# Kernel tuning notes

Measured on AMD Instinct MI355X. Metric: run time of the kernel, lower is better.

The kernel has to match this reference:

```python
import jax, jax.numpy as jnp
import numpy as np

B, IN, H, U = 65536, 128, 256, 256

def lecun_tanh(x):
    return 1.7159 * jnp.tanh(0.666 * x)

def _xavier(key, shape):
    fan_out, fan_in = shape
    limit = np.sqrt(6.0 / (fan_in + fan_out))
    return jax.random.uniform(key, shape, jnp.float32, -limit, limit)

def setup_inputs() -> dict:
    key = jax.random.key(0)
    ks = jax.random.split(key, 12)
    return {
        "input": jax.random.normal(ks[0], (B, IN), jnp.float32),
        "hx": jax.random.normal(ks[1], (B, H), jnp.float32),
        "ts": jax.random.uniform(ks[2], (B, 1), jnp.float32),
        # backbone Linear(IN+H -> U)
        "Wb": _xavier(ks[3], (U, IN + H)),
        "bb": jnp.zeros((U,), jnp.float32),
        # ff1, ff2, time_a, time_b: Linear(U -> H)
        "W1": _xavier(ks[4], (H, U)),
        "b1": jnp.zeros((H,), jnp.float32),
        "W2": _xavier(ks[5], (H, U)),
        "b2": jnp.zeros((H,), jnp.float32),
        "Wa": _xavier(ks[6], (H, U)),
        "ba": jnp.zeros((H,), jnp.float32),
        "Wt": _xavier(ks[7], (H, U)),
        "bt": jnp.zeros((H,), jnp.float32),
    }

def reference(input, hx, ts, Wb, bb, W1, b1, W2, b2, Wa, ba, Wt, bt):
    # x = cat([input, hx]) -> backbone MLP (1 layer, LeCun tanh)
    x = jnp.concatenate([input, hx], axis=1)          # [B, IN+H]
    x = lecun_tanh(x @ Wb.T + bb)                     # [B, U]
    ff1 = jnp.tanh(x @ W1.T + b1)                     # [B, H]
    ff2 = jnp.tanh(x @ W2.T + b2)
    t_a = x @ Wa.T + ba
    t_b = x @ Wt.T + bt
    t_interp = jax.nn.sigmoid(t_a * ts + t_b)         # ts broadcasts [B,1]
    new_hidden = ff1 * (1.0 - t_interp) + t_interp * ff2
    return new_hidden
```

## Files before the change

### kernel.cpp

```cpp
#include <hip/hip_runtime.h>

typedef float v4f __attribute__((ext_vector_type(4)));
typedef short v8s __attribute__((ext_vector_type(8)));

#define BM 64

__device__ __forceinline__ unsigned short f2bf(float f) {
    union { float f; unsigned u; } v; v.f = f;
    unsigned u = v.u;
    u += 0x7FFFu + ((u >> 16) & 1u);
    return (unsigned short)(u >> 16);
}

__device__ __forceinline__ unsigned cvt_pk_bf16(float lo, float hi) {
    unsigned r;
    asm("v_cvt_pk_bf16_f32 %0, %1, %2" : "=v"(r) : "v"(lo), "v"(hi));
    return r;
}

#define LDS_BARRIER() do {                                        \
    asm volatile("s_waitcnt lgkmcnt(0)" ::: "memory");            \
    __builtin_amdgcn_s_barrier();                                 \
    __builtin_amdgcn_sched_barrier(0);                            \
} while (0)

#define SB() __builtin_amdgcn_sched_barrier(0)

__device__ __forceinline__ float fast_exp2(float x) {
#if __has_builtin(__builtin_amdgcn_exp2f)
    return __builtin_amdgcn_exp2f(x);
#else
    return exp2f(x);
#endif
}
__device__ __forceinline__ float fast_rcp(float x) {
#if __has_builtin(__builtin_amdgcn_rcpf)
    return __builtin_amdgcn_rcpf(x);
#else
    return 1.0f / x;
#endif
}
__device__ __forceinline__ float fast_tanh(float y) {
    float t = fast_exp2(y * 2.885390081777927f);
    return (t - 1.0f) * fast_rcp(t + 1.0f);
}
__device__ __forceinline__ float fast_sigmoid(float z) {
    float t = fast_exp2(-1.4426950408889634f * z);
    return fast_rcp(1.0f + t);
}

__global__ void prep_pack(const float* __restrict__ Wb, const float* __restrict__ W1,
                          const float* __restrict__ W2, const float* __restrict__ Wa,
                          const float* __restrict__ Wt, unsigned short* __restrict__ ws)
{
    int e = blockIdx.x * 256 + threadIdx.x;
    if (e >= 360448) return;
    const float* src; int K; int base;
    if (e < 98304)       { src = Wb; K = 384; base = 0; }
    else if (e < 163840) { src = W1; K = 256; base = 98304; }
    else if (e < 229376) { src = W2; K = 256; base = 163840; }
    else if (e < 294912) { src = Wa; K = 256; base = 229376; }
    else                 { src = Wt; K = 256; base = 294912; }
    int le   = e - base;
    int j    = le & 7;
    int lane = (le >> 3) & 63;
    int tile = le >> 9;
    int kt   = K >> 5;
    int ks   = tile % kt;
    int nt   = tile / kt;
    int n = nt * 16 + (lane & 15);
    int k = ks * 32 + (lane >> 4) * 8 + j;
    ws[e] = f2bf(src[n * K + k]);
}

__global__ __launch_bounds__(256, 2) void cfc_fused(
    const float* __restrict__ xin, const float* __restrict__ hx,
    const float* __restrict__ ts,
    const float* __restrict__ bb, const float* __restrict__ b1,
    const float* __restrict__ b2, const float* __restrict__ ba,
    const float* __restrict__ bt,
    const unsigned short* __restrict__ wpk,
    float* __restrict__ out)
{
    __shared__ unsigned short lds[16384];
    const int tid  = threadIdx.x;
    const int lane = tid & 63;
    const int w    = tid >> 6;
    const int row0 = blockIdx.x * BM;

    v8s br0[4], br1[4], br2[4];
    v8s afA[4], afB[4];

#define BLOAD(S, DST) do {                                                    \
    _Pragma("unroll")                                                         \
    for (int i = 0; i < 4; ++i) {                                             \
        size_t goff;                                                          \
        if ((S) < 12) {                                                       \
            goff = (size_t)((w * 4 + i) * 12 + (S)) * 512;                    \
        } else {                                                              \
            int s2_ = (S) - 12, g_ = s2_ >> 3, ks_ = s2_ & 7;                 \
            goff = 98304u + (size_t)i * 65536                                 \
                 + (size_t)((w * 4 + g_) * 8 + ks_) * 512;                    \
        }                                                                     \
        DST[i] = *reinterpret_cast<const v8s*>(wpk + goff + (size_t)lane * 8);\
    }                                                                         \
} while (0)

#define ISSUE_IN(SRC, LD, BUF) do {                                           \
    _Pragma("unroll")                                                         \
    for (int it = 0; it < 8; ++it) {                                          \
        int i_ = tid + it * 256; int r_ = i_ >> 5; int c4_ = i_ & 31;         \
        BUF[it] = *(reinterpret_cast<const v4f*>((SRC) + (size_t)r_ * (LD)) + c4_); \
    }                                                                         \
} while (0)

#define WRITE_IN(BUF) do {                                                    \
    _Pragma("unroll")                                                         \
    for (int it = 0; it < 8; ++it) {                                          \
        int i_ = tid + it * 256; int r_ = i_ >> 5; int c4_ = i_ & 31;         \
        uint2 pk_;                                                            \
        pk_.x = cvt_pk_bf16(BUF[it][0], BUF[it][1]);                          \
        pk_.y = cvt_pk_bf16(BUF[it][2], BUF[it][3]);                          \
        int idx_ = (((r_ >> 4) * 4 + (c4_ >> 3)) * 64 + ((c4_ >> 1) & 3) * 16 \
                    + (r_ & 15)) * 8 + (c4_ & 1) * 4;                         \
        *reinterpret_cast<uint2*>(&lds[idx_]) = pk_;                          \
    }                                                                         \
} while (0)

#define P1STEP(S, CUR, PRE) do {                                              \
    BLOAD((S) + 2, PRE);                                                      \
    v8s aa_[4];                                                               \
    _Pragma("unroll")                                                         \
    for (int mt = 0; mt < 4; ++mt)                                            \
        aa_[mt] = *reinterpret_cast<const v8s*>(                              \
                      &lds[((mt * 4 + ((S) & 3)) * 64 + lane) * 8]);          \
    __builtin_amdgcn_s_setprio(1);                                            \
    _Pragma("unroll")                                                         \
    for (int nt = 0; nt < 4; ++nt)                                            \
        _Pragma("unroll")                                                     \
        for (int mt = 0; mt < 4; ++mt)                                        \
            acc[nt][mt] = __builtin_amdgcn_mfma_f32_16x16x32_bf16(            \
                              aa_[mt], CUR[nt], acc[nt][mt], 0, 0, 0);        \
    __builtin_amdgcn_s_setprio(0);                                            \
    SB();                                                                     \
} while (0)

#define P2STEP(S, KS, CUR, PRE, AC, AP) do {                                  \
    BLOAD((S) + 2, PRE);                                                      \
    _Pragma("unroll")                                                         \
    for (int mt = 0; mt < 4; ++mt)                                            \
        AP[mt] = *reinterpret_cast<const v8s*>(                               \
                     &lds[((mt * 8 + (((KS) + 1) & 7)) * 64 + lane) * 8]);    \
    __builtin_amdgcn_s_setprio(1);                                            \
    _Pragma("unroll")                                                         \
    for (int mat = 0; mat < 4; ++mat)                                         \
        _Pragma("unroll")                                                     \
        for (int mt = 0; mt < 4; ++mt)                                        \
            a2[mat][mt] = __builtin_amdgcn_mfma_f32_16x16x32_bf16(            \
                              AC[mt], CUR[mat], a2[mat][mt], 0, 0, 0);        \
    __builtin_amdgcn_s_setprio(0);                                            \
    SB();                                                                     \
} while (0)

#define P2STEP_NS(S, KS, CUR, AC, AP) do {                                    \
    _Pragma("unroll")                                                         \
    for (int mt = 0; mt < 4; ++mt)                                            \
        AP[mt] = *reinterpret_cast<const v8s*>(                               \
                     &lds[((mt * 8 + (((KS) + 1) & 7)) * 64 + lane) * 8]);    \
    __builtin_amdgcn_s_setprio(1);                                            \
    _Pragma("unroll")                                                         \
    for (int mat = 0; mat < 4; ++mat)                                         \
        _Pragma("unroll")                                                     \
        for (int mt = 0; mt < 4; ++mt)                                        \
            a2[mat][mt] = __builtin_amdgcn_mfma_f32_16x16x32_bf16(            \
                              AC[mt], CUR[mat], a2[mat][mt], 0, 0, 0);        \
    __builtin_amdgcn_s_setprio(0);                                            \
    SB();                                                                     \
} while (0)

#define GINIT(G) do {                                                         \
    const int n_ = w * 64 + (G) * 16 + (lane & 15);                           \
    float v1_ = b1[n_], v2_ = b2[n_], va_ = ba[n_], vt_ = bt[n_];             \
    v4f q1_ = {v1_,v1_,v1_,v1_}, q2_ = {v2_,v2_,v2_,v2_};                     \
    v4f qa_ = {va_,va_,va_,va_}, qt_ = {vt_,vt_,vt_,vt_};                     \
    _Pragma("unroll")                                                         \
    for (int mt = 0; mt < 4; ++mt) {                                          \
        a2[0][mt] = q1_; a2[1][mt] = q2_; a2[2][mt] = qa_; a2[3][mt] = qt_;   \
    }                                                                         \
} while (0)

#define EPI(G) do {                                                           \
    const int n_ = w * 64 + (G) * 16 + (lane & 15);                           \
    _Pragma("unroll")                                                         \
    for (int mt = 0; mt < 4; ++mt) {                                          \
        int rowb_ = row0 + mt * 16 + ((lane >> 4) << 2);                      \
        _Pragma("unroll")                                                     \
        for (int r = 0; r < 4; ++r) {                                         \
            float ff1_ = fast_tanh(a2[0][mt][r]);                             \
            float ff2_ = fast_tanh(a2[1][mt][r]);                             \
            float ti_  = fast_sigmoid(a2[2][mt][r] * tsv4[mt][r] + a2[3][mt][r]); \
            out[(size_t)(rowb_ + r) * 256 + n_] = ff1_ + ti_ * (ff2_ - ff1_); \
        }                                                                     \
    }                                                                         \
} while (0)

    BLOAD(0, br0); BLOAD(1, br1);

    v4f acc[4][4];
    #pragma unroll
    for (int nt = 0; nt < 4; ++nt) {
        float bv = bb[w * 64 + nt * 16 + (lane & 15)];
        v4f bvv = {bv, bv, bv, bv};
        #pragma unroll
        for (int mt = 0; mt < 4; ++mt) acc[nt][mt] = bvv;
    }

    v4f stgA[8], stgB[8];
    ISSUE_IN(xin + (size_t)row0 * 128, 128, stgA);
    WRITE_IN(stgA);
    ISSUE_IN(hx + (size_t)row0 * 256, 256, stgB);
    LDS_BARRIER();
    P1STEP(0, br0, br2); P1STEP(1, br1, br0);
    P1STEP(2, br2, br1); P1STEP(3, br0, br2);
    LDS_BARRIER();
    WRITE_IN(stgB);
    ISSUE_IN(hx + (size_t)row0 * 256 + 128, 256, stgA);
    LDS_BARRIER();
    P1STEP(4, br1, br0); P1STEP(5, br2, br1);
    P1STEP(6, br0, br2); P1STEP(7, br1, br0);
    LDS_BARRIER();
    WRITE_IN(stgA);
    LDS_BARRIER();
    P1STEP(8, br2, br1); P1STEP(9, br0, br2);
    P1STEP(10, br1, br0); P1STEP(11, br2, br1);

    v4f tsv4[4];
    #pragma unroll
    for (int mt = 0; mt < 4; ++mt)
        tsv4[mt] = *reinterpret_cast<const v4f*>(
                       &ts[row0 + mt * 16 + ((lane >> 4) << 2)]);

    LDS_BARRIER();

    #pragma unroll
    for (int nt = 0; nt < 4; ++nt)
        #pragma unroll
        for (int mt = 0; mt < 4; ++mt)
            #pragma unroll
            for (int r = 0; r < 4; ++r) {
                float xv = 1.7159f * fast_tanh(0.666f * acc[nt][mt][r]);
                int idx = ((mt*8 + w*2 + (nt >> 1)) * 64
                           + ((nt & 1)*2 + ((lane >> 3) & 1)) * 16 + (lane >> 4)*4 + r) * 8
                          + (lane & 7);
                lds[idx] = f2bf(xv);
            }
    LDS_BARRIER();

    #pragma unroll
    for (int mt = 0; mt < 4; ++mt)
        afA[mt] = *reinterpret_cast<const v8s*>(&lds[((mt * 8 + 0) * 64 + lane) * 8]);

    v4f a2[4][4];
    GINIT(0);
    P2STEP(12,0, br0, br2, afA, afB); P2STEP(13,1, br1, br0, afB, afA);
    P2STEP(14,2, br2, br1, afA, afB); P2STEP(15,3, br0, br2, afB, afA);
    P2STEP(16,4, br1, br0, afA, afB); P2STEP(17,5, br2, br1, afB, afA);
    P2STEP(18,6, br0, br2, afA, afB); P2STEP(19,7, br1, br0, afB, afA);
    EPI(0);
    GINIT(1);
    P2STEP(20,0, br2, br1, afA, afB); P2STEP(21,1, br0, br2, afB, afA);
    P2STEP(22,2, br1, br0, afA, afB); P2STEP(23,3, br2, br1, afB, afA);
    P2STEP(24,4, br0, br2, afA, afB); P2STEP(25,5, br1, br0, afB, afA);
    P2STEP(26,6, br2, br1, afA, afB); P2STEP(27,7, br0, br2, afB, afA);
    EPI(1);
    GINIT(2);
    P2STEP(28,0, br1, br0, afA, afB); P2STEP(29,1, br2, br1, afB, afA);
    P2STEP(30,2, br0, br2, afA, afB); P2STEP(31,3, br1, br0, afB, afA);
    P2STEP(32,4, br2, br1, afA, afB); P2STEP(33,5, br0, br2, afB, afA);
    P2STEP(34,6, br1, br0, afA, afB); P2STEP(35,7, br2, br1, afB, afA);
    EPI(2);
    GINIT(3);
    P2STEP(36,0, br0, br2, afA, afB); P2STEP(37,1, br1, br0, afB, afA);
    P2STEP(38,2, br2, br1, afA, afB); P2STEP(39,3, br0, br2, afB, afA);
    P2STEP(40,4, br1, br0, afA, afB); P2STEP(41,5, br2, br1, afB, afA);
    P2STEP_NS(42,6, br0, afA, afB);   P2STEP_NS(43,7, br1, afB, afA);
    EPI(3);

#undef BLOAD
#undef ISSUE_IN
#undef WRITE_IN
#undef P1STEP
#undef P2STEP
#undef P2STEP_NS
#undef GINIT
#undef EPI
}

extern "C" void kernel_launch(void* const* d_in, const int* in_sizes, int n_in,
                              void* d_out, int out_size, void* d_ws, size_t ws_size,
                              hipStream_t stream)
{
    const float* xin = (const float*)d_in[0];
    const float* hx  = (const float*)d_in[1];
    const float* ts  = (const float*)d_in[2];
    const float* Wb  = (const float*)d_in[3];
    const float* bb  = (const float*)d_in[4];
    const float* W1  = (const float*)d_in[5];
    const float* b1  = (const float*)d_in[6];
    const float* W2  = (const float*)d_in[7];
    const float* b2  = (const float*)d_in[8];
    const float* Wa  = (const float*)d_in[9];
    const float* ba  = (const float*)d_in[10];
    const float* Wt  = (const float*)d_in[11];
    const float* bt  = (const float*)d_in[12];

    if (ws_size < 360448 * sizeof(unsigned short)) return;
    unsigned short* wpk = (unsigned short*)d_ws;

    prep_pack<<<1408, 256, 0, stream>>>(Wb, W1, W2, Wa, Wt, wpk);
    cfc_fused<<<1024, 256, 0, stream>>>(xin, hx, ts, bb, b1, b2, ba, bt, wpk,
                                        (float*)d_out);
}
```

Baseline: 75.86 us.

## Shrink register footprint to allow three blocks per CU

Raises the launch-bounds occupancy hint from 2 to 3 blocks per CU and cuts register pressure to fit it. Input staging now moves in 64-column chunks with half-size buffers, so there are more LDS barriers between phase-1 steps. Phase-2 A fragments are no longer double-buffered across steps, and the ts values are loaded inside the epilogue instead of being held in registers. The aim is better latency hiding from higher occupancy, at the cost of extra barriers, less LDS-read prefetch and a possible risk of spills.

New measurement: 131.7 us. 1.74x slower.

```diff
diff --git a/kernel.cpp b/kernel.cpp
--- a/kernel.cpp
+++ b/kernel.cpp
@@ -73,7 +73,7 @@
     ws[e] = f2bf(src[n * K + k]);
 }
 
-__global__ __launch_bounds__(256, 2) void cfc_fused(
+__global__ __launch_bounds__(256, 3) void cfc_fused(
     const float* __restrict__ xin, const float* __restrict__ hx,
     const float* __restrict__ ts,
     const float* __restrict__ bb, const float* __restrict__ b1,
@@ -89,7 +89,6 @@
     const int row0 = blockIdx.x * BM;
 
     v8s br0[4], br1[4], br2[4];
-    v8s afA[4], afB[4];
 
 #define BLOAD(S, DST) do {                                                    \
     _Pragma("unroll")                                                         \
@@ -108,20 +107,20 @@
 
 #define ISSUE_IN(SRC, LD, BUF) do {                                           \
     _Pragma("unroll")                                                         \
-    for (int it = 0; it < 8; ++it) {                                          \
-        int i_ = tid + it * 256; int r_ = i_ >> 5; int c4_ = i_ & 31;         \
+    for (int it = 0; it < 4; ++it) {                                          \
+        int i_ = tid + it * 256; int r_ = i_ >> 4; int c4_ = i_ & 15;         \
         BUF[it] = *(reinterpret_cast<const v4f*>((SRC) + (size_t)r_ * (LD)) + c4_); \
     }                                                                         \
 } while (0)
 
 #define WRITE_IN(BUF) do {                                                    \
     _Pragma("unroll")                                                         \
-    for (int it = 0; it < 8; ++it) {                                          \
-        int i_ = tid + it * 256; int r_ = i_ >> 5; int c4_ = i_ & 31;         \
+    for (int it = 0; it < 4; ++it) {                                          \
+        int i_ = tid + it * 256; int r_ = i_ >> 4; int c4_ = i_ & 15;         \
         uint2 pk_;                                                            \
         pk_.x = cvt_pk_bf16(BUF[it][0], BUF[it][1]);                          \
         pk_.y = cvt_pk_bf16(BUF[it][2], BUF[it][3]);                          \
-        int idx_ = (((r_ >> 4) * 4 + (c4_ >> 3)) * 64 + ((c4_ >> 1) & 3) * 16 \
+        int idx_ = (((r_ >> 4) * 2 + (c4_ >> 3)) * 64 + ((c4_ >> 1) & 3) * 16 \
                     + (r_ & 15)) * 8 + (c4_ & 1) * 4;                         \
         *reinterpret_cast<uint2*>(&lds[idx_]) = pk_;                          \
     }                                                                         \
@@ -133,7 +132,7 @@
     _Pragma("unroll")                                                         \
     for (int mt = 0; mt < 4; ++mt)                                            \
         aa_[mt] = *reinterpret_cast<const v8s*>(                              \
-                      &lds[((mt * 4 + ((S) & 3)) * 64 + lane) * 8]);          \
+                      &lds[((mt * 2 + ((S) & 1)) * 64 + lane) * 8]);          \
     __builtin_amdgcn_s_setprio(1);                                            \
     _Pragma("unroll")                                                         \
     for (int nt = 0; nt < 4; ++nt)                                            \
@@ -145,35 +144,37 @@
     SB();                                                                     \
 } while (0)
 
-#define P2STEP(S, KS, CUR, PRE, AC, AP) do {                                  \
+#define P2STEP(S, KS, CUR, PRE) do {                                          \
     BLOAD((S) + 2, PRE);                                                      \
+    v8s aa_[4];                                                               \
     _Pragma("unroll")                                                         \
     for (int mt = 0; mt < 4; ++mt)                                            \
-        AP[mt] = *reinterpret_cast<const v8s*>(                               \
-                     &lds[((mt * 8 + (((KS) + 1) & 7)) * 64 + lane) * 8]);    \
+        aa_[mt] = *reinterpret_cast<const v8s*>(                              \
+                      &lds[((mt * 8 + (KS)) * 64 + lane) * 8]);               \
     __builtin_amdgcn_s_setprio(1);                                            \
     _Pragma("unroll")                                                         \
     for (int mat = 0; mat < 4; ++mat)                                         \
         _Pragma("unroll")                                                     \
         for (int mt = 0; mt < 4; ++mt)                                        \
             a2[mat][mt] = __builtin_amdgcn_mfma_f32_16x16x32_bf16(            \
-                              AC[mt], CUR[mat], a2[mat][mt], 0, 0, 0);        \
+                              aa_[mt], CUR[mat], a2[mat][mt], 0, 0, 0);       \
     __builtin_amdgcn_s_setprio(0);                                            \
     SB();                                                                     \
 } while (0)
 
-#define P2STEP_NS(S, KS, CUR, AC, AP) do {                                    \
+#define P2STEP_NS(S, KS, CUR) do {                                            \
+    v8s aa_[4];                                                               \
     _Pragma("unroll")                                                         \
     for (int mt = 0; mt < 4; ++mt)                                            \
-        AP[mt] = *reinterpret_cast<const v8s*>(                               \
-                     &lds[((mt * 8 + (((KS) + 1) & 7)) * 64 + lane) * 8]);    \
+        aa_[mt] = *reinterpret_cast<const v8s*>(                              \
+                      &lds[((mt * 8 + (KS)) * 64 + lane) * 8]);               \
     __builtin_amdgcn_s_setprio(1);                                            \
     _Pragma("unroll")                                                         \
     for (int mat = 0; mat < 4; ++mat)                                         \
         _Pragma("unroll")                                                     \
         for (int mt = 0; mt < 4; ++mt)                                        \
             a2[mat][mt] = __builtin_amdgcn_mfma_f32_16x16x32_bf16(            \
-                              AC[mt], CUR[mat], a2[mat][mt], 0, 0, 0);        \
+                              aa_[mt], CUR[mat], a2[mat][mt], 0, 0, 0);       \
     __builtin_amdgcn_s_setprio(0);                                            \
     SB();                                                                     \
 } while (0)
@@ -194,17 +195,16 @@
     _Pragma("unroll")                                                         \
     for (int mt = 0; mt < 4; ++mt) {                                          \
         int rowb_ = row0 + mt * 16 + ((lane >> 4) << 2);                      \
+        v4f tsv_ = *reinterpret_cast<const v4f*>(&ts[rowb_]);                 \
         _Pragma("unroll")                                                     \
         for (int r = 0; r < 4; ++r) {                                         \
             float ff1_ = fast_tanh(a2[0][mt][r]);                             \
             float ff2_ = fast_tanh(a2[1][mt][r]);                             \
-            float ti_  = fast_sigmoid(a2[2][mt][r] * tsv4[mt][r] + a2[3][mt][r]); \
+            float ti_  = fast_sigmoid(a2[2][mt][r] * tsv_[r] + a2[3][mt][r]); \
             out[(size_t)(rowb_ + r) * 256 + n_] = ff1_ + ti_ * (ff2_ - ff1_); \
         }                                                                     \
     }                                                                         \
 } while (0)
-
-    BLOAD(0, br0); BLOAD(1, br1);
 
     v4f acc[4][4];
     #pragma unroll
@@ -215,30 +215,37 @@
         for (int mt = 0; mt < 4; ++mt) acc[nt][mt] = bvv;
     }
 
-    v4f stgA[8], stgB[8];
-    ISSUE_IN(xin + (size_t)row0 * 128, 128, stgA);
-    WRITE_IN(stgA);
-    ISSUE_IN(hx + (size_t)row0 * 256, 256, stgB);
+    v4f sA[4], sB[4];
+    ISSUE_IN(xin + (size_t)row0 * 128, 128, sA);
+    BLOAD(0, br0); BLOAD(1, br1);
+    WRITE_IN(sA);
+    ISSUE_IN(xin + (size_t)row0 * 128 + 64, 128, sB);
     LDS_BARRIER();
     P1STEP(0, br0, br2); P1STEP(1, br1, br0);
+    LDS_BARRIER();
+    WRITE_IN(sB);
+    ISSUE_IN(hx + (size_t)row0 * 256, 256, sA);
+    LDS_BARRIER();
     P1STEP(2, br2, br1); P1STEP(3, br0, br2);
     LDS_BARRIER();
-    WRITE_IN(stgB);
-    ISSUE_IN(hx + (size_t)row0 * 256 + 128, 256, stgA);
+    WRITE_IN(sA);
+    ISSUE_IN(hx + (size_t)row0 * 256 + 64, 256, sB);
     LDS_BARRIER();
     P1STEP(4, br1, br0); P1STEP(5, br2, br1);
+    LDS_BARRIER();
+    WRITE_IN(sB);
+    ISSUE_IN(hx + (size_t)row0 * 256 + 128, 256, sA);
+    LDS_BARRIER();
     P1STEP(6, br0, br2); P1STEP(7, br1, br0);
     LDS_BARRIER();
-    WRITE_IN(stgA);
+    WRITE_IN(sA);
+    ISSUE_IN(hx + (size_t)row0 * 256 + 192, 256, sB);
     LDS_BARRIER();
     P1STEP(8, br2, br1); P1STEP(9, br0, br2);
+    LDS_BARRIER();
+    WRITE_IN(sB);
+    LDS_BARRIER();
     P1STEP(10, br1, br0); P1STEP(11, br2, br1);
-
-    v4f tsv4[4];
-    #pragma unroll
-    for (int mt = 0; mt < 4; ++mt)
-        tsv4[mt] = *reinterpret_cast<const v4f*>(
-                       &ts[row0 + mt * 16 + ((lane >> 4) << 2)]);
 
     LDS_BARRIER();
 
@@ -256,34 +263,30 @@
             }
     LDS_BARRIER();
 
-    #pragma unroll
-    for (int mt = 0; mt < 4; ++mt)
-        afA[mt] = *reinterpret_cast<const v8s*>(&lds[((mt * 8 + 0) * 64 + lane) * 8]);
-
     v4f a2[4][4];
     GINIT(0);
-    P2STEP(12,0, br0, br2, afA, afB); P2STEP(13,1, br1, br0, afB, afA);
-    P2STEP(14,2, br2, br1, afA, afB); P2STEP(15,3, br0, br2, afB, afA);
-    P2STEP(16,4, br1, br0, afA, afB); P2STEP(17,5, br2, br1, afB, afA);
-    P2STEP(18,6, br0, br2, afA, afB); P2STEP(19,7, br1, br0, afB, afA);
+    P2STEP(12,0, br0, br2); P2STEP(13,1, br1, br0);
+    P2STEP(14,2, br2, br1); P2STEP(15,3, br0, br2);
+    P2STEP(16,4, br1, br0); P2STEP(17,5, br2, br1);
+    P2STEP(18,6, br0, br2); P2STEP(19,7, br1, br0);
     EPI(0);
     GINIT(1);
-    P2STEP(20,0, br2, br1, afA, afB); P2STEP(21,1, br0, br2, afB, afA);
-    P2STEP(22,2, br1, br0, afA, afB); P2STEP(23,3, br2, br1, afB, afA);
-    P2STEP(24,4, br0, br2, afA, afB); P2STEP(25,5, br1, br0, afB, afA);
-    P2STEP(26,6, br2, br1, afA, afB); P2STEP(27,7, br0, br2, afB, afA);
+    P2STEP(20,0, br2, br1); P2STEP(21,1, br0, br2);
+    P2STEP(22,2, br1, br0); P2STEP(23,3, br2, br1);
+    P2STEP(24,4, br0, br2); P2STEP(25,5, br1, br0);
+    P2STEP(26,6, br2, br1); P2STEP(27,7, br0, br2);
     EPI(1);
     GINIT(2);
-    P2STEP(28,0, br1, br0, afA, afB); P2STEP(29,1, br2, br1, afB, afA);
-    P2STEP(30,2, br0, br2, afA, afB); P2STEP(31,3, br1, br0, afB, afA);
-    P2STEP(32,4, br2, br1, afA, afB); P2STEP(33,5, br0, br2, afB, afA);
-    P2STEP(34,6, br1, br0, afA, afB); P2STEP(35,7, br2, br1, afB, afA);
+    P2STEP(28,0, br1, br0); P2STEP(29,1, br2, br1);
+    P2STEP(30,2, br0, br2); P2STEP(31,3, br1, br0);
+    P2STEP(32,4, br2, br1); P2STEP(33,5, br0, br2);
+    P2STEP(34,6, br1, br0); P2STEP(35,7, br2, br1);
     EPI(2);
     GINIT(3);
-    P2STEP(36,0, br0, br2, afA, afB); P2STEP(37,1, br1, br0, afB, afA);
-    P2STEP(38,2, br2, br1, afA, afB); P2STEP(39,3, br0, br2, afB, afA);
-    P2STEP(40,4, br1, br0, afA, afB); P2STEP(41,5, br2, br1, afB, afA);
-    P2STEP_NS(42,6, br0, afA, afB);   P2STEP_NS(43,7, br1, afB, afA);
+    P2STEP(36,0, br0, br2); P2STEP(37,1, br1, br0);
+    P2STEP(38,2, br2, br1); P2STEP(39,3, br0, br2);
+    P2STEP(40,4, br1, br0); P2STEP(41,5, br2, br1);
+    P2STEP_NS(42,6, br0);   P2STEP_NS(43,7, br1);
     EPI(3);
 
 #undef BLOAD
```
